# Performance work log

Hardware: AMD Instinct MI355X
Metric: run time of the kernel (lower is better)

Reference implementation:

```python
import jax, jax.numpy as jnp
import numpy as np

N_NODES = 100000
AVG_DEG = 16
D_IN, D_HID, D_OUT = 128, 128, 64


def setup_inputs() -> dict:
    key = jax.random.key(0)
    k_x, k_w1, k_w2 = jax.random.split(key, 3)
    rng = np.random.default_rng(0)
    # random adjacency edges + self-loops (I + A)
    src = rng.integers(0, N_NODES, N_NODES * AVG_DEG)
    dst = rng.integers(0, N_NODES, N_NODES * AVG_DEG)
    loops = np.arange(N_NODES)
    src = np.concatenate([src, loops]).astype(np.int32)
    dst = np.concatenate([dst, loops]).astype(np.int32)
    # symmetric normalization D^{-1/2} (I+A) D^{-1/2}; deg = row sums of I+A
    deg = np.bincount(src, minlength=N_NODES).astype(np.float32)
    val = (1.0 / np.sqrt(deg[src] * deg[dst])).astype(np.float32)
    return {
        "x": jax.random.normal(k_x, (N_NODES, D_IN), dtype=jnp.float32),
        "W1": jax.random.normal(k_w1, (D_IN, D_HID), dtype=jnp.float32),
        "W2": jax.random.normal(k_w2, (D_HID, D_OUT), dtype=jnp.float32),
        "edge_src": jnp.asarray(src),
        "edge_dst": jnp.asarray(dst),
        "edge_val": jnp.asarray(val),
    }


def _gcn_layer(x, W, src, dst, val, n):
    xw = x @ W                               # dense GEMM: [N, d_out]
    msg = val[:, None] * xw[dst]             # gather along edges: [E, d_out]
    return jax.ops.segment_sum(msg, src, num_segments=n)  # A_hat @ (XW)


def reference(x, W1, W2, edge_src, edge_dst, edge_val):
    n = x.shape[0]
    h = jax.nn.relu(_gcn_layer(x, W1, edge_src, edge_dst, edge_val, n))
    h = jax.nn.relu(_gcn_layer(h, W2, edge_src, edge_dst, edge_val, n))
    return jax.nn.softmax(h, axis=-1)
```

## Files before the change

### kernel.cpp

```cpp
#include <hip/hip_runtime.h>
#include <hip/hip_fp16.h>
#include <math.h>

#define DHID 128
#define DOUT 64
#define EPB 4096
#define BUCK_SH 8
#define CAP 6656

typedef _Float16 half8 __attribute__((ext_vector_type(8)));
typedef float f32x4 __attribute__((ext_vector_type(4)));

static inline size_t align_up(size_t v, size_t a) { return (v + a - 1) / a * a; }


__global__ __launch_bounds__(256) void k_bincount(const int* __restrict__ src, int* __restrict__ dir,
                                                  int E, int nbuck, int nblka) {
    __shared__ int hist[512];
    int tid = threadIdx.x;
    for (int i = tid; i < nbuck; i += 256) hist[i] = 0;
    __syncthreads();
    int e0 = blockIdx.x * EPB;
    #pragma unroll
    for (int j = 0; j < EPB / 256; ++j) {
        int e = e0 + tid + j * 256;
        if (e < E) atomicAdd(&hist[src[e] >> BUCK_SH], 1);
    }
    __syncthreads();
    for (int i = tid; i < nbuck; i += 256) dir[i * nblka + blockIdx.x] = hist[i];
}

__global__ __launch_bounds__(256) void k_rowsum(const int* __restrict__ dir, int* __restrict__ btot,
                                                int nblka) {
    __shared__ int red[256];
    int tid = threadIdx.x, b = blockIdx.x;
    int s = 0;
    for (int j = tid; j < nblka; j += 256) s += dir[b * nblka + j];
    red[tid] = s; __syncthreads();
    #pragma unroll
    for (int d = 128; d > 0; d >>= 1) {
        if (tid < d) red[tid] += red[tid + d];
        __syncthreads();
    }
    if (tid == 0) btot[b] = red[0];
}

__global__ __launch_bounds__(256) void k_dirscan(int* __restrict__ dir, const int* __restrict__ btot,
                                                 int* __restrict__ bucketbase, int* __restrict__ off,
                                                 int n, int nbuck, int nblka, int E) {
    __shared__ int h[512], s4[128], redb[256];
    int tid = threadIdx.x, b = blockIdx.x;
    int s = 0;
    for (int i = tid; i < b; i += 256) s += btot[i];
    redb[tid] = s; __syncthreads();
    #pragma unroll
    for (int d = 128; d > 0; d >>= 1) {
        if (tid < d) redb[tid] += redb[tid + d];
        __syncthreads();
    }
    int base = redb[0];
    if (tid == 0) {
        bucketbase[b] = base;
        if (b == 0) off[n] = E;
        if (b == nbuck - 1) bucketbase[nbuck] = E;
    }
    for (int j = tid; j < nblka; j += 256) h[j] = dir[b * nblka + j];
    __syncthreads();
    int nq = (nblka + 3) >> 2;
    if (tid < nq) {
        int t = 0;
        #pragma unroll
        for (int j = 0; j < 4; ++j) { int idx = tid * 4 + j; if (idx < nblka) t += h[idx]; }
        s4[tid] = t;
    }
    __syncthreads();
    if (tid == 0) { int run = 0; for (int i = 0; i < nq; ++i) { int t = s4[i]; s4[i] = run; run += t; } }
    __syncthreads();
    if (tid < nq) {
        int run = s4[tid] + base;
        #pragma unroll
        for (int j = 0; j < 4; ++j) {
            int idx = tid * 4 + j;
            if (idx < nblka) { int t = h[idx]; dir[b * nblka + idx] = run; run += t; }
        }
    }
}

__global__ __launch_bounds__(256) void k_binwrite(const int* __restrict__ src, const int* __restrict__ dst,
                                                  const float* __restrict__ val, const int* __restrict__ dir,
                                                  int2* __restrict__ cpair, int E, int nbuck, int nblka) {
    __shared__ int skey[EPB], sdst[EPB], sval[EPB];
    __shared__ int hist[512], hbase[512], s4[128];
    int tid = threadIdx.x, blk = blockIdx.x;
    int e0 = blk * EPB;
    int cnt = E - e0; if (cnt > EPB) cnt = EPB;

    for (int i = tid; i < nbuck; i += 256) hist[i] = 0;
    __syncthreads();
    #pragma unroll
    for (int j = 0; j < EPB / 256; ++j) {
        int e = e0 + tid + j * 256;
        if (e < E) atomicAdd(&hist[src[e] >> BUCK_SH], 1);
    }
    __syncthreads();
    int nq = (nbuck + 3) >> 2;
    if (tid < nq) {
        int s = 0;
        #pragma unroll
        for (int j = 0; j < 4; ++j) { int idx = tid * 4 + j; if (idx < nbuck) s += hist[idx]; }
        s4[tid] = s;
    }
    __syncthreads();
    if (tid == 0) { int run = 0; for (int i = 0; i < nq; ++i) { int t = s4[i]; s4[i] = run; run += t; } }
    __syncthreads();
    if (tid < nq) {
        int run = s4[tid];
        #pragma unroll
        for (int j = 0; j < 4; ++j) {
            int idx = tid * 4 + j;
            if (idx < nbuck) { hbase[idx] = run; run += hist[idx]; }
        }
    }
    __syncthreads();
    for (int i = tid; i < nbuck; i += 256) hist[i] = hbase[i];
    __syncthreads();
    #pragma unroll
    for (int j = 0; j < EPB / 256; ++j) {
        int e = e0 + tid + j * 256;
        if (e < E) {
            int s = src[e];
            int bk = s >> BUCK_SH;
            int p = atomicAdd(&hist[bk], 1);
            skey[p] = s;
            sdst[p] = dst[e];
            sval[p] = __float_as_int(val[e]);
        }
    }
    __syncthreads();
    for (int i = tid; i < cnt; i += 256) {
        int s = skey[i];
        int bk = s >> BUCK_SH;
        int gb = dir[bk * nblka + blk];
        int lr = i - hbase[bk];
        cpair[gb + lr] = make_int2(((s & 255) << 17) | sdst[i], sval[i]);
    }
}

__global__ __launch_bounds__(256) void k_csrify(const int* __restrict__ bucketbase, int2* __restrict__ cpair,
                                                int* __restrict__ off, int n) {
    __shared__ int2 sp[CAP];
    __shared__ int h[256], loff[256], cur[256], s4[64];
    int tid = threadIdx.x, b = blockIdx.x;
    int base = bucketbase[b];
    int cnt = bucketbase[b + 1] - base;
    if (cnt > CAP) cnt = CAP;
    for (int i = tid; i < cnt; i += 256) sp[i] = cpair[base + i];
    h[tid] = 0;
    __syncthreads();
    for (int i = tid; i < cnt; i += 256) atomicAdd(&h[sp[i].x >> 17], 1);
    __syncthreads();
    if (tid < 64) {
        int s = 0;
        #pragma unroll
        for (int j = 0; j < 4; ++j) s += h[tid * 4 + j];
        s4[tid] = s;
    }
    __syncthreads();
    if (tid == 0) { int run = 0; for (int i = 0; i < 64; ++i) { int t = s4[i]; s4[i] = run; run += t; } }
    __syncthreads();
    if (tid < 64) {
        int run = s4[tid];
        #pragma unroll
        for (int j = 0; j < 4; ++j) { int idx = tid * 4 + j; loff[idx] = run; run += h[idx]; }
    }
    __syncthreads();
    int node0 = b << BUCK_SH;
    int nodes_b = n - node0; if (nodes_b > 256) nodes_b = 256;
    if (tid < nodes_b) off[node0 + tid] = base + loff[tid];
    cur[tid] = loff[tid];
    __syncthreads();
    for (int i = tid; i < cnt; i += 256) {
        int sl = sp[i].x >> 17;
        int p = atomicAdd(&cur[sl], 1);
        cpair[base + p] = make_int2(sp[i].x & 0x1FFFF, sp[i].y);
    }
}

__global__ __launch_bounds__(256) void k_wprep(const float* __restrict__ W1, const float* __restrict__ W2,
                                               _Float16* __restrict__ Wt1, _Float16* __restrict__ Wt2) {
    int b = blockIdx.x, tid = threadIdx.x;
    if (b < 64) {
        int m = b * 256 + tid;
        int c = m >> 7, k = m & 127;
        Wt1[m] = (_Float16)W1[(size_t)k * 128 + c];
    } else {
        int m = (b - 64) * 256 + tid;
        int c = m >> 7, k = m & 127;
        Wt2[m] = (_Float16)W2[(size_t)k * 64 + c];
    }
}

__global__ __launch_bounds__(256) void k_gemm1(const float* __restrict__ x, const _Float16* __restrict__ Wt1,
                                               __half* __restrict__ xw, int n) {
    __shared__ _Float16 Ws[128 * 128];
    int tid = threadIdx.x;
    int row0 = blockIdx.x * 64;

    #pragma unroll
    for (int m0 = 0; m0 < 2048; m0 += 256) {
        int m = tid + m0;
        int c = m >> 4, kq = m & 15;
        uint4 v = *(const uint4*)(Wt1 + (size_t)m * 8);
        int byte = (c * 256 + kq * 16) ^ ((c & 7) << 4);
        *(uint4*)((char*)Ws + byte) = v;
    }
    __syncthreads();

    int lane = tid & 63;
    int wid = tid >> 6;
    int rg = row0 + wid * 16 + (lane & 15); if (rg >= n) rg = n - 1;
    int kgrp = (lane >> 4) * 8;

    f32x4 acc[8];
    #pragma unroll
    for (int t = 0; t < 8; ++t) acc[t] = (f32x4){0.f, 0.f, 0.f, 0.f};

    #pragma unroll
    for (int kk = 0; kk < 128; kk += 32) {
        int ks = kk + kgrp;
        const float4* xp = (const float4*)(x + (size_t)rg * 128 + ks);
        float4 f0 = xp[0], f1 = xp[1];
        half8 a;
        a[0] = (_Float16)f0.x; a[1] = (_Float16)f0.y; a[2] = (_Float16)f0.z; a[3] = (_Float16)f0.w;
        a[4] = (_Float16)f1.x; a[5] = (_Float16)f1.y; a[6] = (_Float16)f1.z; a[7] = (_Float16)f1.w;
        #pragma unroll
        for (int t = 0; t < 8; ++t) {
            int c = t * 16 + (lane & 15);
            int bbyte = (c * 256 + ks * 2) ^ ((c & 7) << 4);
            half8 b = *(const half8*)((const char*)Ws + bbyte);
            acc[t] = __builtin_amdgcn_mfma_f32_16x16x32_f16(a, b, acc[t], 0, 0, 0);
        }
    }

    #pragma unroll
    for (int t = 0; t < 8; ++t) {
        int c = t * 16 + (lane & 15);
        #pragma unroll
        for (int j = 0; j < 4; ++j) {
            int rs = row0 + wid * 16 + (lane >> 4) * 4 + j;
            if (rs < n) xw[(size_t)rs * 128 + c] = __float2half(acc[t][j]);
        }
    }
}

__global__ __launch_bounds__(256) void k_gemm2(const __half* __restrict__ h1, const _Float16* __restrict__ Wt2,
                                               __half* __restrict__ hw, int n) {
    __shared__ _Float16 Ws[64 * 128];
    int tid = threadIdx.x;
    int row0 = blockIdx.x * 64;

    #pragma unroll
    for (int m0 = 0; m0 < 1024; m0 += 256) {
        int m = tid + m0;
        int c = m >> 4, kq = m & 15;
        uint4 v = *(const uint4*)(Wt2 + (size_t)m * 8);
        int byte = (c * 256 + kq * 16) ^ ((c & 7) << 4);
        *(uint4*)((char*)Ws + byte) = v;
    }
    __syncthreads();

    int lane = tid & 63;
    int wid = tid >> 6;
    int rg = row0 + wid * 16 + (lane & 15); if (rg >= n) rg = n - 1;
    int kgrp = (lane >> 4) * 8;

    f32x4 acc[4];
    #pragma unroll
    for (int t = 0; t < 4; ++t) acc[t] = (f32x4){0.f, 0.f, 0.f, 0.f};

    #pragma unroll
    for (int kk = 0; kk < 128; kk += 32) {
        int ks = kk + kgrp;
        half8 a = *(const half8*)((const void*)(h1 + (size_t)rg * 128 + ks));
        #pragma unroll
        for (int t = 0; t < 4; ++t) {
            int c = t * 16 + (lane & 15);
            int bbyte = (c * 256 + ks * 2) ^ ((c & 7) << 4);
            half8 b = *(const half8*)((const char*)Ws + bbyte);
            acc[t] = __builtin_amdgcn_mfma_f32_16x16x32_f16(a, b, acc[t], 0, 0, 0);
        }
    }

    #pragma unroll
    for (int t = 0; t < 4; ++t) {
        int c = t * 16 + (lane & 15);
        #pragma unroll
        for (int j = 0; j < 4; ++j) {
            int rs = row0 + wid * 16 + (lane >> 4) * 4 + j;
            if (rs < n) hw[(size_t)rs * 64 + c] = __float2half(acc[t][j]);
        }
    }
}

__global__ __launch_bounds__(256) void k_agg1(const __half* __restrict__ xw, const int* __restrict__ off,
                                              const int2* __restrict__ cpair,
                                              __half* __restrict__ h1, int n) {
    int wave = threadIdx.x >> 6;
    int lane = threadIdx.x & 63;
    int node = blockIdx.x * 4 + wave;
    if (node >= n) return;
    int s = off[node], e = off[node + 1];
    float ax = 0.f, ay = 0.f;
    int i = s;
    for (; i + 8 <= e; i += 8) {
        int2 p[8];
        #pragma unroll
        for (int j = 0; j < 8; ++j) p[j] = cpair[i + j];
        float2 v[8];
        #pragma unroll
        for (int j = 0; j < 8; ++j)
            v[j] = __half22float2(((const __half2*)(xw + (size_t)p[j].x * 128))[lane]);
        #pragma unroll
        for (int j = 0; j < 8; ++j) {
            float w = __int_as_float(p[j].y);
            ax += w * v[j].x; ay += w * v[j].y;
        }
    }
    for (; i + 4 <= e; i += 4) {
        int2 p[4];
        #pragma unroll
        for (int j = 0; j < 4; ++j) p[j] = cpair[i + j];
        float2 v[4];
        #pragma unroll
        for (int j = 0; j < 4; ++j)
            v[j] = __half22float2(((const __half2*)(xw + (size_t)p[j].x * 128))[lane]);
        #pragma unroll
        for (int j = 0; j < 4; ++j) {
            float w = __int_as_float(p[j].y);
            ax += w * v[j].x; ay += w * v[j].y;
        }
    }
    for (; i < e; ++i) {
        int2 p = cpair[i];
        float w = __int_as_float(p.y);
        float2 v = __half22float2(((const __half2*)(xw + (size_t)p.x * 128))[lane]);
        ax += w * v.x; ay += w * v.y;
    }
    ((__half2*)(h1 + (size_t)node * 128))[lane] = __floats2half2_rn(fmaxf(ax, 0.f), fmaxf(ay, 0.f));
}

__global__ __launch_bounds__(256) void k_agg2(const __half* __restrict__ hw, const int* __restrict__ off,
                                              const int2* __restrict__ cpair,
                                              float* __restrict__ out, int n) {
    int wave = threadIdx.x >> 6;
    int lane = threadIdx.x & 63;
    int node = blockIdx.x * 4 + wave;
    if (node >= n) return;
    int s = off[node], e = off[node + 1];
    float acc = 0.f;
    int i = s;
    for (; i + 8 <= e; i += 8) {
        int2 p[8];
        #pragma unroll
        for (int j = 0; j < 8; ++j) p[j] = cpair[i + j];
        float v[8];
        #pragma unroll
        for (int j = 0; j < 8; ++j)
            v[j] = __half2float(hw[(size_t)p[j].x * 64 + lane]);
        #pragma unroll
        for (int j = 0; j < 8; ++j)
            acc += __int_as_float(p[j].y) * v[j];
    }
    for (; i + 4 <= e; i += 4) {
        int2 p[4];
        #pragma unroll
        for (int j = 0; j < 4; ++j) p[j] = cpair[i + j];
        float v[4];
        #pragma unroll
        for (int j = 0; j < 4; ++j)
            v[j] = __half2float(hw[(size_t)p[j].x * 64 + lane]);
        #pragma unroll
        for (int j = 0; j < 4; ++j)
            acc += __int_as_float(p[j].y) * v[j];
    }
    for (; i < e; ++i) {
        int2 p = cpair[i];
        acc += __int_as_float(p.y) * __half2float(hw[(size_t)p.x * 64 + lane]);
    }
    acc = fmaxf(acc, 0.f);
    float m = acc;
    #pragma unroll
    for (int o = 32; o > 0; o >>= 1) m = fmaxf(m, __shfl_xor(m, o));
    float ex = expf(acc - m);
    float sum = ex;
    #pragma unroll
    for (int o = 32; o > 0; o >>= 1) sum += __shfl_xor(sum, o);
    out[(size_t)node * 64 + lane] = ex / sum;
}

extern "C" void kernel_launch(void* const* d_in, const int* in_sizes, int n_in,
                              void* d_out, int out_size, void* d_ws, size_t ws_size,
                              hipStream_t stream) {
    const float* x = (const float*)d_in[0];
    const float* W1 = (const float*)d_in[1];
    const float* W2 = (const float*)d_in[2];
    const int* esrc = (const int*)d_in[3];
    const int* edst = (const int*)d_in[4];
    const float* evalv = (const float*)d_in[5];
    int n = in_sizes[0] / DHID;
    int E = in_sizes[3];

    int nbuck = (n + 255) >> BUCK_SH;
    int nblka = (E + EPB - 1) / EPB;

    char* p = (char*)d_ws;
    int* off = (int*)p;        p += align_up((size_t)(n + 1) * 4, 256);
    int* bucketbase = (int*)p; p += align_up((size_t)(nbuck + 1) * 4, 256);
    int* btot = (int*)p;       p += align_up((size_t)nbuck * 4, 256);
    int* dir = (int*)p;        p += align_up((size_t)nbuck * nblka * 4, 256);
    int2* cpair = (int2*)p;    p += align_up((size_t)E * 8, 256);
    _Float16* Wt1 = (_Float16*)p; p += align_up((size_t)128 * 128 * 2, 256);
    _Float16* Wt2 = (_Float16*)p; p += align_up((size_t)64 * 128 * 2, 256);
    __half* xw = (__half*)p;   p += align_up((size_t)n * DHID * 2, 256);
    __half* h1 = (__half*)p;   p += align_up((size_t)n * DHID * 2, 256);
    __half* hw2 = xw;

    k_wprep<<<96, 256, 0, stream>>>(W1, W2, Wt1, Wt2);
    k_gemm1<<<(n + 63) / 64, 256, 0, stream>>>(x, Wt1, xw, n);
    k_bincount<<<nblka, 256, 0, stream>>>(esrc, dir, E, nbuck, nblka);
    k_rowsum<<<nbuck, 256, 0, stream>>>(dir, btot, nblka);
    k_dirscan<<<nbuck, 256, 0, stream>>>(dir, btot, bucketbase, off, n, nbuck, nblka, E);
    k_binwrite<<<nblka, 256, 0, stream>>>(esrc, edst, evalv, dir, cpair, E, nbuck, nblka);
    k_csrify<<<nbuck, 256, 0, stream>>>(bucketbase, cpair, off, n);
    k_agg1<<<(n + 3) / 4, 256, 0, stream>>>(xw, off, cpair, h1, n);
    k_gemm2<<<(n + 63) / 64, 256, 0, stream>>>(h1, Wt2, hw2, n);
    k_agg2<<<(n + 3) / 4, 256, 0, stream>>>(hw2, off, cpair, (float*)d_out, n);
}
```

Measured before the change: 211.4 us.

## Simplify edge binning: drop rowsum kernel, scatter directly via global atomics

Bucket totals are now accumulated by global atomics inside the bincount kernel, with zeroing folded into the weight-prep kernel, which removes the separate rowsum launch. The binwrite kernel no longer re-histograms and stages edges in shared memory; it scatters each edge straight to global memory using per-block cursors seeded from the scanned directory. The csrify kernel reads from a separate temporary buffer instead of staging a bucket in shared memory, which also removes the CAP overflow truncation. The cost is less coalesced scattered writes, an extra E*8-byte workspace buffer, and repeated global reads in csrify.

```diff
diff --git a/kernel.cpp b/kernel.cpp
--- a/kernel.cpp
+++ b/kernel.cpp
@@ -6,7 +6,6 @@
 #define DOUT 64
 #define EPB 4096
 #define BUCK_SH 8
-#define CAP 6656
 
 typedef _Float16 half8 __attribute__((ext_vector_type(8)));
 typedef float f32x4 __attribute__((ext_vector_type(4)));
@@ -15,7 +14,7 @@
 
 
 __global__ __launch_bounds__(256) void k_bincount(const int* __restrict__ src, int* __restrict__ dir,
-                                                  int E, int nbuck, int nblka) {
+                                                  int* __restrict__ btot, int E, int nbuck, int nblka) {
     __shared__ int hist[512];
     int tid = threadIdx.x;
     for (int i = tid; i < nbuck; i += 256) hist[i] = 0;
@@ -27,22 +26,11 @@
         if (e < E) atomicAdd(&hist[src[e] >> BUCK_SH], 1);
     }
     __syncthreads();
-    for (int i = tid; i < nbuck; i += 256) dir[i * nblka + blockIdx.x] = hist[i];
-}
-
-__global__ __launch_bounds__(256) void k_rowsum(const int* __restrict__ dir, int* __restrict__ btot,
-                                                int nblka) {
-    __shared__ int red[256];
-    int tid = threadIdx.x, b = blockIdx.x;
-    int s = 0;
-    for (int j = tid; j < nblka; j += 256) s += dir[b * nblka + j];
-    red[tid] = s; __syncthreads();
-    #pragma unroll
-    for (int d = 128; d > 0; d >>= 1) {
-        if (tid < d) red[tid] += red[tid + d];
-        __syncthreads();
-    }
-    if (tid == 0) btot[b] = red[0];
+    for (int i = tid; i < nbuck; i += 256) {
+        int c = hist[i];
+        dir[i * nblka + blockIdx.x] = c;
+        if (c) atomicAdd(&btot[i], c);
+    }
 }
 
 __global__ __launch_bounds__(256) void k_dirscan(int* __restrict__ dir, const int* __restrict__ btot,
@@ -88,76 +76,34 @@
 
 __global__ __launch_bounds__(256) void k_binwrite(const int* __restrict__ src, const int* __restrict__ dst,
                                                   const float* __restrict__ val, const int* __restrict__ dir,
-                                                  int2* __restrict__ cpair, int E, int nbuck, int nblka) {
-    __shared__ int skey[EPB], sdst[EPB], sval[EPB];
-    __shared__ int hist[512], hbase[512], s4[128];
+                                                  int2* __restrict__ ctmp, int E, int nbuck, int nblka) {
+    __shared__ int cur[512];
     int tid = threadIdx.x, blk = blockIdx.x;
+    for (int i = tid; i < nbuck; i += 256) cur[i] = dir[i * nblka + blk];
+    __syncthreads();
     int e0 = blk * EPB;
-    int cnt = E - e0; if (cnt > EPB) cnt = EPB;
-
-    for (int i = tid; i < nbuck; i += 256) hist[i] = 0;
-    __syncthreads();
-    #pragma unroll
-    for (int j = 0; j < EPB / 256; ++j) {
-        int e = e0 + tid + j * 256;
-        if (e < E) atomicAdd(&hist[src[e] >> BUCK_SH], 1);
-    }
-    __syncthreads();
-    int nq = (nbuck + 3) >> 2;
-    if (tid < nq) {
-        int s = 0;
-        #pragma unroll
-        for (int j = 0; j < 4; ++j) { int idx = tid * 4 + j; if (idx < nbuck) s += hist[idx]; }
-        s4[tid] = s;
-    }
-    __syncthreads();
-    if (tid == 0) { int run = 0; for (int i = 0; i < nq; ++i) { int t = s4[i]; s4[i] = run; run += t; } }
-    __syncthreads();
-    if (tid < nq) {
-        int run = s4[tid];
-        #pragma unroll
-        for (int j = 0; j < 4; ++j) {
-            int idx = tid * 4 + j;
-            if (idx < nbuck) { hbase[idx] = run; run += hist[idx]; }
-        }
-    }
-    __syncthreads();
-    for (int i = tid; i < nbuck; i += 256) hist[i] = hbase[i];
-    __syncthreads();
     #pragma unroll
     for (int j = 0; j < EPB / 256; ++j) {
         int e = e0 + tid + j * 256;
         if (e < E) {
             int s = src[e];
             int bk = s >> BUCK_SH;
-            int p = atomicAdd(&hist[bk], 1);
-            skey[p] = s;
-            sdst[p] = dst[e];
-            sval[p] = __float_as_int(val[e]);
-        }
-    }
-    __syncthreads();
-    for (int i = tid; i < cnt; i += 256) {
-        int s = skey[i];
-        int bk = s >> BUCK_SH;
-        int gb = dir[bk * nblka + blk];
-        int lr = i - hbase[bk];
-        cpair[gb + lr] = make_int2(((s & 255) << 17) | sdst[i], sval[i]);
-    }
-}
-
-__global__ __launch_bounds__(256) void k_csrify(const int* __restrict__ bucketbase, int2* __restrict__ cpair,
+            int p = atomicAdd(&cur[bk], 1);
+            ctmp[p] = make_int2(((s & 255) << 17) | dst[e], __float_as_int(val[e]));
+        }
+    }
+}
+
+__global__ __launch_bounds__(256) void k_csrify(const int* __restrict__ bucketbase,
+                                                const int2* __restrict__ ctmp, int2* __restrict__ cpair,
                                                 int* __restrict__ off, int n) {
-    __shared__ int2 sp[CAP];
     __shared__ int h[256], loff[256], cur[256], s4[64];
     int tid = threadIdx.x, b = blockIdx.x;
     int base = bucketbase[b];
     int cnt = bucketbase[b + 1] - base;
-    if (cnt > CAP) cnt = CAP;
-    for (int i = tid; i < cnt; i += 256) sp[i] = cpair[base + i];
     h[tid] = 0;
     __syncthreads();
-    for (int i = tid; i < cnt; i += 256) atomicAdd(&h[sp[i].x >> 17], 1);
+    for (int i = tid; i < cnt; i += 256) atomicAdd(&h[ctmp[base + i].x >> 17], 1);
     __syncthreads();
     if (tid < 64) {
         int s = 0;
@@ -180,15 +126,19 @@
     cur[tid] = loff[tid];
     __syncthreads();
     for (int i = tid; i < cnt; i += 256) {
-        int sl = sp[i].x >> 17;
+        int2 v = ctmp[base + i];
+        int sl = v.x >> 17;
         int p = atomicAdd(&cur[sl], 1);
-        cpair[base + p] = make_int2(sp[i].x & 0x1FFFF, sp[i].y);
+        cpair[base + p] = make_int2(v.x & 0x1FFFF, v.y);
     }
 }
 
 __global__ __launch_bounds__(256) void k_wprep(const float* __restrict__ W1, const float* __restrict__ W2,
-                                               _Float16* __restrict__ Wt1, _Float16* __restrict__ Wt2) {
+                                               _Float16* __restrict__ Wt1, _Float16* __restrict__ Wt2,
+                                               int* __restrict__ btot, int nbuck) {
     int b = blockIdx.x, tid = threadIdx.x;
+    int gid = b * 256 + tid;
+    if (gid < nbuck) btot[gid] = 0;
     if (b < 64) {
         int m = b * 256 + tid;
         int c = m >> 7, k = m & 127;
@@ -418,6 +368,7 @@
     int* bucketbase = (int*)p; p += align_up((size_t)(nbuck + 1) * 4, 256);
     int* btot = (int*)p;       p += align_up((size_t)nbuck * 4, 256);
     int* dir = (int*)p;        p += align_up((size_t)nbuck * nblka * 4, 256);
+    int2* ctmp = (int2*)p;     p += align_up((size_t)E * 8, 256);
     int2* cpair = (int2*)p;    p += align_up((size_t)E * 8, 256);
     _Float16* Wt1 = (_Float16*)p; p += align_up((size_t)128 * 128 * 2, 256);
     _Float16* Wt2 = (_Float16*)p; p += align_up((size_t)64 * 128 * 2, 256);
@@ -425,13 +376,12 @@
     __half* h1 = (__half*)p;   p += align_up((size_t)n * DHID * 2, 256);
     __half* hw2 = xw;
 
-    k_wprep<<<96, 256, 0, stream>>>(W1, W2, Wt1, Wt2);
+    k_wprep<<<96, 256, 0, stream>>>(W1, W2, Wt1, Wt2, btot, nbuck);
     k_gemm1<<<(n + 63) / 64, 256, 0, stream>>>(x, Wt1, xw, n);
-    k_bincount<<<nblka, 256, 0, stream>>>(esrc, dir, E, nbuck, nblka);
-    k_rowsum<<<nbuck, 256, 0, stream>>>(dir, btot, nblka);
+    k_bincount<<<nblka, 256, 0, stream>>>(esrc, dir, btot, E, nbuck, nblka);
     k_dirscan<<<nbuck, 256, 0, stream>>>(dir, btot, bucketbase, off, n, nbuck, nblka, E);
-    k_binwrite<<<nblka, 256, 0, stream>>>(esrc, edst, evalv, dir, cpair, E, nbuck, nblka);
-    k_csrify<<<nbuck, 256, 0, stream>>>(bucketbase, cpair, off, n);
+    k_binwrite<<<nblka, 256, 0, stream>>>(esrc, edst, evalv, dir, ctmp, E, nbuck, nblka);
+    k_csrify<<<nbuck, 256, 0, stream>>>(bucketbase, ctmp, cpair, off, n);
     k_agg1<<<(n + 3) / 4, 256, 0, stream>>>(xw, off, cpair, h1, n);
     k_gemm2<<<(n + 63) / 64, 256, 0, stream>>>(h1, Wt2, hw2, n);
     k_agg2<<<(n + 3) / 4, 256, 0, stream>>>(hw2, off, cpair, (float*)d_out, n);
```

After: 212.3 us. Within noise of the previous version (+0.4%).
